# Performance work log

Measured on AMD Instinct MI355X. Metric: run time of the kernel, lower is better.

Reference implementation:

```python
import jax, jax.numpy as jnp
import numpy as np
from jax import lax

VOCAB = 1000
TMAX = 1001  # max_episode_length + 1
L = 2048
H_GRU = 256


def setup_inputs() -> dict:
    key = jax.random.key(0)
    ks = jax.random.split(key, 40)
    g = lambda i, shape, s: jax.random.normal(ks[i], shape, dtype=jnp.float32) * s
    inp = {
        "x": jax.random.normal(ks[0], (1, 3, 124, 124), dtype=jnp.float32),
        "curr_instr": jax.random.randint(ks[1], (1, L), 0, VOCAB),
        "prev_instr": jax.random.randint(ks[2], (1, L), 0, VOCAB),
        "next_instr": jax.random.randint(ks[3], (1, L), 0, VOCAB),
        "tx": jax.random.randint(ks[4], (1,), 0, TMAX),
        "hx": jnp.zeros((1, 768), jnp.float32),
        "cx": jnp.zeros((1, 768), jnp.float32),
        # conv stack
        "conv1_w": g(5, (128, 3, 8, 8), 0.05), "conv1_b": jnp.zeros((128,), jnp.float32),
        "conv2_w": g(6, (64, 128, 4, 4), 0.03), "conv2_b": jnp.zeros((64,), jnp.float32),
        "conv3_w": g(7, (64, 64, 4, 4), 0.03), "conv3_b": jnp.zeros((64,), jnp.float32),
        # embeddings
        "emb": g(8, (VOCAB, 32), 0.1),
        "time_emb": g(9, (TMAX, 32), 0.1),
        # GRU (torch nn.GRU layout: 3*H rows for r,z,n)
        "gru_w_ih": g(10, (3 * H_GRU, 32), 0.1), "gru_w_hh": g(11, (3 * H_GRU, H_GRU), 0.06),
        "gru_b_ih": jnp.zeros((3 * H_GRU,), jnp.float32), "gru_b_hh": jnp.zeros((3 * H_GRU,), jnp.float32),
        # attention linear 256 -> 64
        "attn_w": g(12, (64, H_GRU), 0.06), "attn_b": jnp.zeros((64,), jnp.float32),
        # image-fusion linear 64*6*6 -> 256
        "lin_w": g(13, (256, 64 * 6 * 6), 0.02), "lin_b": jnp.zeros((256,), jnp.float32),
        # LSTMCell 768 -> 768 (torch layout: 4*H rows for i,f,g,o)
        "lstm_w_ih": g(14, (4 * 768, 768), 0.03), "lstm_w_hh": g(15, (4 * 768, 768), 0.03),
        "lstm_b_ih": jnp.zeros((4 * 768,), jnp.float32), "lstm_b_hh": jnp.zeros((4 * 768,), jnp.float32),
        # heads over [hx, time_emb] = 768 + 32 = 800
        "critic_w": g(16, (1, 800), 0.03), "critic_b": jnp.zeros((1,), jnp.float32),
        "actor_w": g(17, (4, 800), 0.01), "actor_b": jnp.zeros((4,), jnp.float32),
    }
    return inp


def _conv(x, w, b, s):
    return lax.conv_general_dilated(x, w, (s, s), "VALID") + b[None, :, None, None]


def reference(x, curr_instr, prev_instr, next_instr, tx, hx, cx,
              conv1_w, conv1_b, conv2_w, conv2_b, conv3_w, conv3_b,
              emb, time_emb, gru_w_ih, gru_w_hh, gru_b_ih, gru_b_hh,
              attn_w, attn_b, lin_w, lin_b,
              lstm_w_ih, lstm_w_hh, lstm_b_ih, lstm_b_hh,
              critic_w, critic_b, actor_w, actor_b):
    # image tower: [1,3,124,124] -> [1,64,6,6]
    h1 = jax.nn.relu(_conv(x, conv1_w, conv1_b, 4))
    h2 = jax.nn.relu(_conv(h1, conv2_w, conv2_b, 2))
    x_image_rep = jax.nn.relu(_conv(h2, conv3_w, conv3_b, 2))

    # three instruction sequences, encoded by a shared GRU (vmapped scan)
    tokens = jnp.stack([curr_instr[0], prev_instr[0], next_instr[0]])  # [3, L]

    def gru_encode(tok):
        xs = emb[tok]                               # [L, 32]
        gi_all = xs @ gru_w_ih.T + gru_b_ih         # precompute input gates [L, 3H]
        def step(h, gi):
            gh = h @ gru_w_hh.T + gru_b_hh
            i_r, i_z, i_n = jnp.split(gi, 3)
            h_r, h_z, h_n = jnp.split(gh, 3)
            r = jax.nn.sigmoid(i_r + h_r)
            z = jax.nn.sigmoid(i_z + h_z)
            n = jnp.tanh(i_n + r * h_n)
            return (1.0 - z) * n + z * h, None
        h, _ = lax.scan(step, jnp.zeros((H_GRU,), xs.dtype), gi_all)
        return h

    h3 = jax.vmap(gru_encode)(tokens)               # [3, 256]
    attn = jax.nn.sigmoid(h3 @ attn_w.T + attn_b)   # [3, 64]

    # BUG-FAITHFUL: original forward uses cached_computation['curr_x_attention']
    # for all three branches, so the three fused features are identical.
    curr_attn = attn[0][None, :, None, None]        # [1,64,1,1]
    fused = (x_image_rep * curr_attn).reshape(1, -1)  # [1, 2304]
    feat = jax.nn.relu(fused @ lin_w.T + lin_b)     # [1, 256]
    xcat = jnp.concatenate([feat, feat, feat], axis=1)  # [1, 768]

    # LSTMCell
    gates = xcat @ lstm_w_ih.T + lstm_b_ih + hx @ lstm_w_hh.T + lstm_b_hh  # [1, 3072]
    gi, gf, gg, go = jnp.split(gates, 4, axis=1)
    cx_new = jax.nn.sigmoid(gf) * cx + jax.nn.sigmoid(gi) * jnp.tanh(gg)
    hx_new = jax.nn.sigmoid(go) * jnp.tanh(cx_new)

    t = time_emb[tx].reshape(-1, 32)                # [1, 32]
    z = jnp.concatenate([hx_new, t], axis=1)        # [1, 800]
    critic = z @ critic_w.T + critic_b              # [1, 1]
    actor = z @ actor_w.T + actor_b                 # [1, 4]
    return critic, actor, hx_new, cx_new
```

## Files before the change

kernel.cpp:

```cpp
#include <hip/hip_runtime.h>
#include <hip/hip_bf16.h>
#include <stdint.h>


typedef _Float16 half8 __attribute__((ext_vector_type(8)));
typedef _Float16 half2v __attribute__((ext_vector_type(2)));
typedef float f32x4 __attribute__((ext_vector_type(4)));

__device__ __forceinline__ float sigm(float x) { return 1.0f / (1.0f + __expf(-x)); }
__device__ __forceinline__ float tanh_f(float x) { return 2.0f / (1.0f + __expf(-2.0f * x)) - 1.0f; }

__global__ void k_pack(const float* __restrict__ whh, uint32_t* __restrict__ wf16p) {
    int i = blockIdx.x * 256 + threadIdx.x;
    if (i >= 98304) return;
    half2v p = {(_Float16)whh[2 * i], (_Float16)whh[2 * i + 1]};
    wf16p[i] = __builtin_bit_cast(uint32_t, p);
}

__global__ void k_conv1(const float* __restrict__ x, const float* __restrict__ w,
                        const float* __restrict__ b, float* __restrict__ h1) {
    int idx = blockIdx.x * 256 + threadIdx.x;
    if (idx >= 128 * 30 * 30) return;
    int ox = idx % 30, oy = (idx / 30) % 30, oc = idx / 900;
    const float* wr = w + oc * 192;
    float acc = b[oc];
    for (int c = 0; c < 3; ++c)
        for (int ky = 0; ky < 8; ++ky) {
            const float* xr = x + (c * 124 + oy * 4 + ky) * 124 + ox * 4;
            const float* wk = wr + (c * 8 + ky) * 8;
#pragma unroll
            for (int kx = 0; kx < 8; ++kx) acc = fmaf(xr[kx], wk[kx], acc);
        }
    h1[idx] = fmaxf(acc, 0.0f);
}

__global__ void k_conv2(const float* __restrict__ h1, const float* __restrict__ w,
                        const float* __restrict__ b, float* __restrict__ h2) {
    int idx = blockIdx.x * 256 + threadIdx.x;
    if (idx >= 64 * 14 * 14) return;
    int ox = idx % 14, oy = (idx / 14) % 14, oc = idx / 196;
    float acc = b[oc];
    const float* wr = w + oc * 128 * 16;
    for (int c = 0; c < 128; ++c) {
#pragma unroll
        for (int ky = 0; ky < 4; ++ky) {
            const float* hr = h1 + (c * 30 + oy * 2 + ky) * 30 + ox * 2;
            const float* wk = wr + (c * 4 + ky) * 4;
#pragma unroll
            for (int kx = 0; kx < 4; ++kx) acc = fmaf(hr[kx], wk[kx], acc);
        }
    }
    h2[idx] = fmaxf(acc, 0.0f);
}

__global__ void k_conv3(const float* __restrict__ h2, const float* __restrict__ w,
                        const float* __restrict__ b, float* __restrict__ x3) {
    int idx = blockIdx.x * 256 + threadIdx.x;
    if (idx >= 64 * 6 * 6) return;
    int ox = idx % 6, oy = (idx / 6) % 6, oc = idx / 36;
    float acc = b[oc];
    const float* wr = w + oc * 64 * 16;
    for (int c = 0; c < 64; ++c) {
#pragma unroll
        for (int ky = 0; ky < 4; ++ky) {
            const float* hr = h2 + (c * 14 + oy * 2 + ky) * 14 + ox * 2;
            const float* wk = wr + (c * 4 + ky) * 4;
#pragma unroll
            for (int kx = 0; kx < 4; ++kx) acc = fmaf(hr[kx], wk[kx], acc);
        }
    }
    x3[idx] = fmaxf(acc, 0.0f);
}

__global__ void k_gi(const int* __restrict__ curr, const float* __restrict__ emb,
                     const float* __restrict__ wih, const float* __restrict__ bih,
                     const float* __restrict__ bhh, float* __restrict__ gi) {
    int idx = blockIdx.x * 256 + threadIdx.x;
    int j = idx % 768, t = idx / 768;
    int tok = curr[t];
    const float4* e = (const float4*)(emb + tok * 32);
    const float4* wr = (const float4*)(wih + j * 32);
    float acc = bih[j] + (j < 512 ? bhh[j] : 0.0f);
#pragma unroll
    for (int k = 0; k < 8; ++k) {
        float4 ev = e[k], wv = wr[k];
        acc = fmaf(ev.x, wv.x, acc);
        acc = fmaf(ev.y, wv.y, acc);
        acc = fmaf(ev.z, wv.z, acc);
        acc = fmaf(ev.w, wv.w, acc);
    }
    gi[idx] = acc;
}

#define DECLBT(T) uint4 b##T##_0, b##T##_1, b##T##_2, b##T##_3, b##T##_4, b##T##_5, b##T##_6, b##T##_7;
#define LOADBK(T, kt, off) b##T##_##kt = wpR[(off) + (kt)*4 + quad];
#define LOADBT(T, off) LOADBK(T, 0, off) LOADBK(T, 1, off) LOADBK(T, 2, off) LOADBK(T, 3, off) \
                       LOADBK(T, 4, off) LOADBK(T, 5, off) LOADBK(T, 6, off) LOADBK(T, 7, off)
#define TIEBK(T, kt) \
    asm volatile("" : "+v"(b##T##_##kt.x), "+v"(b##T##_##kt.y), "+v"(b##T##_##kt.z), "+v"(b##T##_##kt.w));
#define TIEBT(T) TIEBK(T, 0) TIEBK(T, 1) TIEBK(T, 2) TIEBK(T, 3) TIEBK(T, 4) TIEBK(T, 5) TIEBK(T, 6) TIEBK(T, 7)
#define MF1(T, kt, areg) \
    acc##T = __builtin_amdgcn_mfma_f32_16x16x32_f16(areg, __builtin_bit_cast(half8, b##T##_##kt), acc##T, 0, 0, 0);
#define MFK(kt, areg) MF1(0, kt, areg) MF1(1, kt, areg) MF1(2, kt, areg) \
                      MF1(3, kt, areg) MF1(4, kt, areg) MF1(5, kt, areg)

__global__ __attribute__((amdgpu_flat_work_group_size(512, 512), amdgpu_waves_per_eu(2, 2)))
void k_gru_scan(const float* __restrict__ gi, const uint32_t* __restrict__ wf16p,
                const float* __restrict__ bhh, const float* __restrict__ attn_w,
                const float* __restrict__ attn_b, float* __restrict__ attn0) {
    __shared__ __align__(16) _Float16 hbuf[1024];
    const int tid = threadIdx.x;
    const int lane = tid & 63;
    const int wv = tid >> 6;
    const int n16 = lane & 15;
    const int quad = lane >> 4;
    const int li = n16;

    DECLBT(0) DECLBT(1) DECLBT(2) DECLBT(3) DECLBT(4) DECLBT(5)
    {
        const uint4* wpR = (const uint4*)wf16p + (size_t)(wv * 32 + n16) * 32;
        LOADBT(0, 0) LOADBT(1, 512) LOADBT(2, 8192) LOADBT(3, 8704) LOADBT(4, 16384) LOADBT(5, 16896)
    }
    TIEBT(0) TIEBT(1) TIEBT(2) TIEBT(3) TIEBT(4) TIEBT(5)

    const float bn0 = bhh[512 + wv * 32 + li];
    const float bn1 = bhh[512 + wv * 32 + 16 + li];
    float gr0, gr1, gz0, gz1, gn0v, gn1v;
    {
        const float* g0 = gi + wv * 32 + li;
        gr0 = g0[0]; gr1 = g0[16]; gz0 = g0[256]; gz1 = g0[272]; gn0v = g0[512]; gn1v = g0[528];
    }
    float h0 = 0.0f, h1 = 0.0f;
    hbuf[tid] = (_Float16)0.0f;
    hbuf[512 + tid] = (_Float16)0.0f;
    __syncthreads();

#pragma clang loop unroll(disable)
    for (int step = 0; step < 2048; ++step) {
        const uint4* ab = (const uint4*)hbuf + ((step & 1) << 6) + ((n16 == 1) ? 4 : 0);
        half8 aA = __builtin_bit_cast(half8, ab[0 * 8 + quad]);
        half8 aB = __builtin_bit_cast(half8, ab[1 * 8 + quad]);

        float pr0 = 0.f, pr1 = 0.f, pz0 = 0.f, pz1 = 0.f, pn0 = 0.f, pn1 = 0.f;
        if (step < 2047) {
            const float* gp = gi + (size_t)(step + 1) * 768 + wv * 32 + li;
            pr0 = gp[0]; pr1 = gp[16]; pz0 = gp[256]; pz1 = gp[272]; pn0 = gp[512]; pn1 = gp[528];
        }

        f32x4 acc0 = (f32x4)(0.0f), acc1 = (f32x4)(0.0f), acc2 = (f32x4)(0.0f);
        f32x4 acc3 = (f32x4)(0.0f), acc4 = (f32x4)(0.0f), acc5 = (f32x4)(0.0f);
        MFK(0, aA) aA = __builtin_bit_cast(half8, ab[2 * 8 + quad]);
        MFK(1, aB) aB = __builtin_bit_cast(half8, ab[3 * 8 + quad]);
        MFK(2, aA) aA = __builtin_bit_cast(half8, ab[4 * 8 + quad]);
        MFK(3, aB) aB = __builtin_bit_cast(half8, ab[5 * 8 + quad]);
        MFK(4, aA) aA = __builtin_bit_cast(half8, ab[6 * 8 + quad]);
        MFK(5, aB) aB = __builtin_bit_cast(half8, ab[7 * 8 + quad]);
        MFK(6, aA)
        MFK(7, aB)

        if (lane < 16) {
            const float SC = 0.0009765625f;
            float yr0 = fmaf(acc0.y, SC, acc0.x);
            float yr1 = fmaf(acc1.y, SC, acc1.x);
            float yz0 = fmaf(acc2.y, SC, acc2.x);
            float yz1 = fmaf(acc3.y, SC, acc3.x);
            float yn0 = fmaf(acc4.y, SC, acc4.x) + bn0;
            float yn1 = fmaf(acc5.y, SC, acc5.x) + bn1;
            float r0 = sigm(gr0 + yr0), r1 = sigm(gr1 + yr1);
            float z0 = sigm(gz0 + yz0), z1 = sigm(gz1 + yz1);
            float n0 = tanh_f(fmaf(r0, yn0, gn0v));
            float n1 = tanh_f(fmaf(r1, yn1, gn1v));
            h0 = fmaf(z0, h0 - n0, n0);
            h1 = fmaf(z1, h1 - n1, n1);
            int wb = (((step + 1) & 1) << 9) + (wv << 6);
            _Float16 h0h = (_Float16)h0, h1h = (_Float16)h1;
            hbuf[wb + li] = h0h;
            hbuf[wb + 32 + li] = (_Float16)((h0 - (float)h0h) * 1024.0f);
            hbuf[wb + 16 + li] = h1h;
            hbuf[wb + 48 + li] = (_Float16)((h1 - (float)h1h) * 1024.0f);
        }
        gr0 = pr0; gr1 = pr1; gz0 = pz0; gz1 = pz1; gn0v = pn0; gn1v = pn1;
        __syncthreads();
    }

    if (tid < 64) {
        const float* ar = attn_w + tid * 256;
        float acc = attn_b[tid];
        for (int k = 0; k < 256; ++k) {
            int c = k >> 5, i = k & 31;
            float hk = (float)hbuf[c * 64 + i] + (float)hbuf[c * 64 + 32 + i] * 0.0009765625f;
            acc = fmaf(ar[k], hk, acc);
        }
        attn0[tid] = sigm(acc);
    }
}

__global__ void k_feat(const float* __restrict__ x3, const float* __restrict__ attn0,
                       const float* __restrict__ lw, const float* __restrict__ lb,
                       float* __restrict__ feat) {
    __shared__ __align__(16) float fused[2304];
    int t = threadIdx.x;
    for (int i = t; i < 2304; i += 64) fused[i] = x3[i] * attn0[i / 36];
    __syncthreads();
    int row = blockIdx.x * 64 + t;
    const float4* wvv = (const float4*)(lw + (size_t)row * 2304);
    float acc = lb[row];
    for (int i = 0; i < 576; ++i) {
        float4 v = wvv[i];
        const float* f = fused + i * 4;
        acc = fmaf(v.x, f[0], acc);
        acc = fmaf(v.y, f[1], acc);
        acc = fmaf(v.z, f[2], acc);
        acc = fmaf(v.w, f[3], acc);
    }
    feat[row] = fmaxf(acc, 0.0f);
}

__global__ void k_lstm_gates(const float* __restrict__ wih, const float* __restrict__ whh,
                             const float* __restrict__ bih, const float* __restrict__ bhh,
                             const float* __restrict__ hx, const float* __restrict__ feat,
                             float* __restrict__ gates) {
    int wid = threadIdx.x >> 6, lane = threadIdx.x & 63;
    int row = blockIdx.x * 4 + wid;
    const float* wi = wih + (size_t)row * 768;
    const float* wh = whh + (size_t)row * 768;
    float acc = 0.0f;
#pragma unroll
    for (int i = 0; i < 12; ++i) {
        int k = lane + i * 64;
        acc = fmaf(wi[k], feat[k & 255], acc);
        acc = fmaf(wh[k], hx[k], acc);
    }
#pragma unroll
    for (int s = 32; s; s >>= 1) acc += __shfl_down(acc, s, 64);
    if (lane == 0) gates[row] = acc + bih[row] + bhh[row];
}

__global__ void k_lstm_cell(const float* __restrict__ gates, const float* __restrict__ cx,
                            float* __restrict__ out, float* __restrict__ hxf) {
    int i = threadIdx.x;
    float g_i = gates[i], g_f = gates[768 + i], g_g = gates[1536 + i], g_o = gates[2304 + i];
    float c = cx[i];
    float cn = sigm(g_f) * c + sigm(g_i) * tanh_f(g_g);
    float hn = sigm(g_o) * tanh_f(cn);
    out[5 + i] = hn;
    out[5 + 768 + i] = cn;
    hxf[i] = hn;
}

__global__ void k_heads(const float* __restrict__ hxf, const float* __restrict__ temb,
                        const int* __restrict__ tx, const float* __restrict__ cw,
                        const float* __restrict__ cb, const float* __restrict__ aw,
                        const float* __restrict__ ab, float* __restrict__ out) {
    __shared__ float z[800];
    int t = threadIdx.x;
    for (int i = t; i < 768; i += 320) z[i] = hxf[i];
    if (t < 32) z[768 + t] = temb[tx[0] * 32 + t];
    __syncthreads();
    int w = t >> 6, lane = t & 63;
    const float* row = (w == 0) ? cw : (aw + (size_t)(w - 1) * 800);
    float acc = 0.0f;
    for (int k = lane; k < 800; k += 64) acc = fmaf(row[k], z[k], acc);
#pragma unroll
    for (int s = 32; s; s >>= 1) acc += __shfl_down(acc, s, 64);
    if (lane == 0) {
        float b = (w == 0) ? cb[0] : ab[w - 1];
        out[w] = acc + b;
    }
}

extern "C" void kernel_launch(void* const* d_in, const int* in_sizes, int n_in,
                              void* d_out, int out_size, void* d_ws, size_t ws_size,
                              hipStream_t stream) {
    const float* x = (const float*)d_in[0];
    const int* curr = (const int*)d_in[1];
    const int* tx = (const int*)d_in[4];
    const float* hx = (const float*)d_in[5];
    const float* cx = (const float*)d_in[6];
    const float* c1w = (const float*)d_in[7];
    const float* c1b = (const float*)d_in[8];
    const float* c2w = (const float*)d_in[9];
    const float* c2b = (const float*)d_in[10];
    const float* c3w = (const float*)d_in[11];
    const float* c3b = (const float*)d_in[12];
    const float* emb = (const float*)d_in[13];
    const float* temb = (const float*)d_in[14];
    const float* gwih = (const float*)d_in[15];
    const float* gwhh = (const float*)d_in[16];
    const float* gbih = (const float*)d_in[17];
    const float* gbhh = (const float*)d_in[18];
    const float* attw = (const float*)d_in[19];
    const float* attb = (const float*)d_in[20];
    const float* linw = (const float*)d_in[21];
    const float* linb = (const float*)d_in[22];
    const float* lwih = (const float*)d_in[23];
    const float* lwhh = (const float*)d_in[24];
    const float* lbih = (const float*)d_in[25];
    const float* lbhh = (const float*)d_in[26];
    const float* cw = (const float*)d_in[27];
    const float* cb = (const float*)d_in[28];
    const float* aw = (const float*)d_in[29];
    const float* ab = (const float*)d_in[30];
    float* out = (float*)d_out;

    char* ws = (char*)d_ws;
    float* gi = (float*)(ws + 0);
    float* h1 = (float*)(ws + 6291456);
    float* h2 = (float*)(ws + 6752256);
    float* x3 = (float*)(ws + 6802432);
    float* attn0 = (float*)(ws + 6811648);
    float* feat = (float*)(ws + 6811904);
    float* gates = (float*)(ws + 6812928);
    float* hxf = (float*)(ws + 6825216);
    uint32_t* wf16p = (uint32_t*)(ws + 6828288);

    k_pack<<<384, 256, 0, stream>>>(gwhh, wf16p);
    k_gi<<<6144, 256, 0, stream>>>(curr, emb, gwih, gbih, gbhh, gi);
    k_conv1<<<450, 256, 0, stream>>>(x, c1w, c1b, h1);
    k_conv2<<<49, 256, 0, stream>>>(h1, c2w, c2b, h2);
    k_conv3<<<9, 256, 0, stream>>>(h2, c3w, c3b, x3);
    k_gru_scan<<<1, 512, 0, stream>>>(gi, wf16p, gbhh, attw, attb, attn0);
    k_feat<<<4, 64, 0, stream>>>(x3, attn0, linw, linb, feat);
    k_lstm_gates<<<768, 256, 0, stream>>>(lwih, lwhh, lbih, lbhh, hx, feat, gates);
    k_lstm_cell<<<1, 768, 0, stream>>>(gates, cx, out, hxf);
    k_heads<<<1, 320, 0, stream>>>(hxf, temb, tx, cw, cb, aw, ab, out);
}
```

Measured before the change: 2.671 ms.

## Split GRU scan across MFMA and dot2 waves; fold conv stack and packing into scan

The GRU recurrence is repartitioned so that four waves compute 128 hidden units with MFMA while the other four waves compute the remaining 128 units with packed fp16 dot2 instructions. Each wave's share of the recurrent matmul per step shrinks. The fp16 weight packing now happens in-kernel from the fp32 weights, which removes the separate pack kernel. The three conv kernels run inside a second block of the same launch, concurrently with the scan, which removes four launches. The risks are higher register pressure (48 uint4 per thread), a wave imbalance between the MFMA and dot2 paths, and a conv stack that is slow on a single block, though it overlaps the long scan.

```diff
diff --git a/kernel.cpp b/kernel.cpp
--- a/kernel.cpp
+++ b/kernel.cpp
@@ -9,68 +9,21 @@
 
 __device__ __forceinline__ float sigm(float x) { return 1.0f / (1.0f + __expf(-x)); }
 __device__ __forceinline__ float tanh_f(float x) { return 2.0f / (1.0f + __expf(-2.0f * x)) - 1.0f; }
-
-__global__ void k_pack(const float* __restrict__ whh, uint32_t* __restrict__ wf16p) {
-    int i = blockIdx.x * 256 + threadIdx.x;
-    if (i >= 98304) return;
-    half2v p = {(_Float16)whh[2 * i], (_Float16)whh[2 * i + 1]};
-    wf16p[i] = __builtin_bit_cast(uint32_t, p);
-}
-
-__global__ void k_conv1(const float* __restrict__ x, const float* __restrict__ w,
-                        const float* __restrict__ b, float* __restrict__ h1) {
-    int idx = blockIdx.x * 256 + threadIdx.x;
-    if (idx >= 128 * 30 * 30) return;
-    int ox = idx % 30, oy = (idx / 30) % 30, oc = idx / 900;
-    const float* wr = w + oc * 192;
-    float acc = b[oc];
-    for (int c = 0; c < 3; ++c)
-        for (int ky = 0; ky < 8; ++ky) {
-            const float* xr = x + (c * 124 + oy * 4 + ky) * 124 + ox * 4;
-            const float* wk = wr + (c * 8 + ky) * 8;
-#pragma unroll
-            for (int kx = 0; kx < 8; ++kx) acc = fmaf(xr[kx], wk[kx], acc);
-        }
-    h1[idx] = fmaxf(acc, 0.0f);
-}
-
-__global__ void k_conv2(const float* __restrict__ h1, const float* __restrict__ w,
-                        const float* __restrict__ b, float* __restrict__ h2) {
-    int idx = blockIdx.x * 256 + threadIdx.x;
-    if (idx >= 64 * 14 * 14) return;
-    int ox = idx % 14, oy = (idx / 14) % 14, oc = idx / 196;
-    float acc = b[oc];
-    const float* wr = w + oc * 128 * 16;
-    for (int c = 0; c < 128; ++c) {
-#pragma unroll
-        for (int ky = 0; ky < 4; ++ky) {
-            const float* hr = h1 + (c * 30 + oy * 2 + ky) * 30 + ox * 2;
-            const float* wk = wr + (c * 4 + ky) * 4;
-#pragma unroll
-            for (int kx = 0; kx < 4; ++kx) acc = fmaf(hr[kx], wk[kx], acc);
-        }
-    }
-    h2[idx] = fmaxf(acc, 0.0f);
-}
-
-__global__ void k_conv3(const float* __restrict__ h2, const float* __restrict__ w,
-                        const float* __restrict__ b, float* __restrict__ x3) {
-    int idx = blockIdx.x * 256 + threadIdx.x;
-    if (idx >= 64 * 6 * 6) return;
-    int ox = idx % 6, oy = (idx / 6) % 6, oc = idx / 36;
-    float acc = b[oc];
-    const float* wr = w + oc * 64 * 16;
-    for (int c = 0; c < 64; ++c) {
-#pragma unroll
-        for (int ky = 0; ky < 4; ++ky) {
-            const float* hr = h2 + (c * 14 + oy * 2 + ky) * 14 + ox * 2;
-            const float* wk = wr + (c * 4 + ky) * 4;
-#pragma unroll
-            for (int kx = 0; kx < 4; ++kx) acc = fmaf(hr[kx], wk[kx], acc);
-        }
-    }
-    x3[idx] = fmaxf(acc, 0.0f);
-}
+__device__ __forceinline__ uint32_t pk(float a, float b) {
+    half2v h = {(_Float16)a, (_Float16)b};
+    return __builtin_bit_cast(uint32_t, h);
+}
+#if __has_builtin(__builtin_amdgcn_fdot2)
+__device__ __forceinline__ float dot2(uint32_t w, uint32_t h, float acc) {
+    return __builtin_amdgcn_fdot2(__builtin_bit_cast(half2v, w),
+                                  __builtin_bit_cast(half2v, h), acc, false);
+}
+#else
+__device__ __forceinline__ float dot2(uint32_t w, uint32_t h, float acc) {
+    half2v wv = __builtin_bit_cast(half2v, w), hv = __builtin_bit_cast(half2v, h);
+    return fmaf((float)wv.y, (float)hv.y, fmaf((float)wv.x, (float)hv.x, acc));
+}
+#endif
 
 __global__ void k_gi(const int* __restrict__ curr, const float* __restrict__ emb,
                      const float* __restrict__ wih, const float* __restrict__ bih,
@@ -92,94 +45,270 @@
     gi[idx] = acc;
 }
 
-#define DECLBT(T) uint4 b##T##_0, b##T##_1, b##T##_2, b##T##_3, b##T##_4, b##T##_5, b##T##_6, b##T##_7;
-#define LOADBK(T, kt, off) b##T##_##kt = wpR[(off) + (kt)*4 + quad];
-#define LOADBT(T, off) LOADBK(T, 0, off) LOADBK(T, 1, off) LOADBK(T, 2, off) LOADBK(T, 3, off) \
-                       LOADBK(T, 4, off) LOADBK(T, 5, off) LOADBK(T, 6, off) LOADBK(T, 7, off)
-#define TIEBK(T, kt) \
-    asm volatile("" : "+v"(b##T##_##kt.x), "+v"(b##T##_##kt.y), "+v"(b##T##_##kt.z), "+v"(b##T##_##kt.w));
-#define TIEBT(T) TIEBK(T, 0) TIEBK(T, 1) TIEBK(T, 2) TIEBK(T, 3) TIEBK(T, 4) TIEBK(T, 5) TIEBK(T, 6) TIEBK(T, 7)
-#define MF1(T, kt, areg) \
-    acc##T = __builtin_amdgcn_mfma_f32_16x16x32_f16(areg, __builtin_bit_cast(half8, b##T##_##kt), acc##T, 0, 0, 0);
-#define MFK(kt, areg) MF1(0, kt, areg) MF1(1, kt, areg) MF1(2, kt, areg) \
-                      MF1(3, kt, areg) MF1(4, kt, areg) MF1(5, kt, areg)
+#define REPU(X) X(0) X(1) X(2) X(3) X(4) X(5) X(6) X(7) X(8) X(9) X(10) X(11)   \
+    X(12) X(13) X(14) X(15) X(16) X(17) X(18) X(19) X(20) X(21) X(22) X(23)     \
+    X(24) X(25) X(26) X(27) X(28) X(29) X(30) X(31) X(32) X(33) X(34) X(35)     \
+    X(36) X(37) X(38) X(39) X(40) X(41) X(42) X(43) X(44) X(45) X(46) X(47)
+#define DECLU(i) uint4 U##i;
+#define TIEU(i) asm volatile("" : "+v"(U##i.x), "+v"(U##i.y), "+v"(U##i.z), "+v"(U##i.w));
+#define PACK8(dst, p)                                  \
+    {                                                  \
+        float4 fA = *(const float4*)(p);               \
+        float4 fB = *(const float4*)((p) + 4);         \
+        dst.x = pk(fA.x, fA.y); dst.y = pk(fA.z, fA.w); \
+        dst.z = pk(fB.x, fB.y); dst.w = pk(fB.z, fB.w); \
+    }
+#define PACKT(u0, u1, u2, u3, u4, u5, u6, u7, rp)                        \
+    PACK8(u0, (rp) + 0 * 32 + quad * 8) PACK8(u1, (rp) + 1 * 32 + quad * 8) \
+    PACK8(u2, (rp) + 2 * 32 + quad * 8) PACK8(u3, (rp) + 3 * 32 + quad * 8) \
+    PACK8(u4, (rp) + 4 * 32 + quad * 8) PACK8(u5, (rp) + 5 * 32 + quad * 8) \
+    PACK8(u6, (rp) + 6 * 32 + quad * 8) PACK8(u7, (rp) + 7 * 32 + quad * 8)
+#define MM(A, B, C) __builtin_amdgcn_mfma_f32_16x16x32_f16(A, __builtin_bit_cast(half8, B), C, 0, 0, 0)
+#define MF6(A, u0, u1, u2, u3, u4, u5)                           \
+    acc0 = MM(A, u0, acc0); acc1 = MM(A, u1, acc1);              \
+    acc2 = MM(A, u2, acc2); acc3 = MM(A, u3, acc3);              \
+    acc4 = MM(A, u4, acc4); acc5 = MM(A, u5, acc5);
+#define CHUNK(cc, A0, A1, A2, A3, B0, B1)                                          \
+    {                                                                              \
+        uint4 hh0 = hb[cc * 8 + 0], hh1 = hb[cc * 8 + 1];                          \
+        uint4 hh2 = hb[cc * 8 + 2], hh3 = hb[cc * 8 + 3];                          \
+        uint4 hl0 = hb[cc * 8 + 4], hl1 = hb[cc * 8 + 5];                          \
+        uint4 hl2 = hb[cc * 8 + 6], hl3 = hb[cc * 8 + 7];                          \
+        uint4 bh0 = hb[cc * 8 + hoff], bh1 = hb[cc * 8 + hoff + 1];                \
+        uint4 bl0 = hb[cc * 8 + hoff + 4], bl1 = hb[cc * 8 + hoff + 5];            \
+        accAH = dot2(A0.x, hh0.x, accAH); accAH = dot2(A0.y, hh0.y, accAH);        \
+        accAH = dot2(A0.z, hh0.z, accAH); accAH = dot2(A0.w, hh0.w, accAH);        \
+        accAH = dot2(A1.x, hh1.x, accAH); accAH = dot2(A1.y, hh1.y, accAH);        \
+        accAH = dot2(A1.z, hh1.z, accAH); accAH = dot2(A1.w, hh1.w, accAH);        \
+        accAH = dot2(A2.x, hh2.x, accAH); accAH = dot2(A2.y, hh2.y, accAH);        \
+        accAH = dot2(A2.z, hh2.z, accAH); accAH = dot2(A2.w, hh2.w, accAH);        \
+        accAH = dot2(A3.x, hh3.x, accAH); accAH = dot2(A3.y, hh3.y, accAH);        \
+        accAH = dot2(A3.z, hh3.z, accAH); accAH = dot2(A3.w, hh3.w, accAH);        \
+        accAL = dot2(A0.x, hl0.x, accAL); accAL = dot2(A0.y, hl0.y, accAL);        \
+        accAL = dot2(A0.z, hl0.z, accAL); accAL = dot2(A0.w, hl0.w, accAL);        \
+        accAL = dot2(A1.x, hl1.x, accAL); accAL = dot2(A1.y, hl1.y, accAL);        \
+        accAL = dot2(A1.z, hl1.z, accAL); accAL = dot2(A1.w, hl1.w, accAL);        \
+        accAL = dot2(A2.x, hl2.x, accAL); accAL = dot2(A2.y, hl2.y, accAL);        \
+        accAL = dot2(A2.z, hl2.z, accAL); accAL = dot2(A2.w, hl2.w, accAL);        \
+        accAL = dot2(A3.x, hl3.x, accAL); accAL = dot2(A3.y, hl3.y, accAL);        \
+        accAL = dot2(A3.z, hl3.z, accAL); accAL = dot2(A3.w, hl3.w, accAL);        \
+        accBH = dot2(B0.x, bh0.x, accBH); accBH = dot2(B0.y, bh0.y, accBH);        \
+        accBH = dot2(B0.z, bh0.z, accBH); accBH = dot2(B0.w, bh0.w, accBH);        \
+        accBH = dot2(B1.x, bh1.x, accBH); accBH = dot2(B1.y, bh1.y, accBH);        \
+        accBH = dot2(B1.z, bh1.z, accBH); accBH = dot2(B1.w, bh1.w, accBH);        \
+        accBL = dot2(B0.x, bl0.x, accBL); accBL = dot2(B0.y, bl0.y, accBL);        \
+        accBL = dot2(B0.z, bl0.z, accBL); accBL = dot2(B0.w, bl0.w, accBL);        \
+        accBL = dot2(B1.x, bl1.x, accBL); accBL = dot2(B1.y, bl1.y, accBL);        \
+        accBL = dot2(B1.z, bl1.z, accBL); accBL = dot2(B1.w, bl1.w, accBL);        \
+    }
 
 __global__ __attribute__((amdgpu_flat_work_group_size(512, 512), amdgpu_waves_per_eu(2, 2)))
-void k_gru_scan(const float* __restrict__ gi, const uint32_t* __restrict__ wf16p,
-                const float* __restrict__ bhh, const float* __restrict__ attn_w,
-                const float* __restrict__ attn_b, float* __restrict__ attn0) {
-    __shared__ __align__(16) _Float16 hbuf[1024];
+void k_scan(const float* __restrict__ gi, const float* __restrict__ whh,
+            const float* __restrict__ bhh, const float* __restrict__ attn_w,
+            const float* __restrict__ attn_b, float* __restrict__ attn0,
+            const float* __restrict__ x, const float* __restrict__ c1w,
+            const float* __restrict__ c1b, const float* __restrict__ c2w,
+            const float* __restrict__ c2b, const float* __restrict__ c3w,
+            const float* __restrict__ c3b, float* __restrict__ h1,
+            float* __restrict__ h2, float* __restrict__ x3) {
+    const int bid = blockIdx.x;
     const int tid = threadIdx.x;
+
+    if (bid == 1) {
+        for (int it = 0; it < 225; ++it) {
+            int idx = it * 512 + tid;
+            int ox = idx % 30, oy = (idx / 30) % 30, oc = idx / 900;
+            const float* wr = c1w + oc * 192;
+            float acc = c1b[oc];
+            for (int c = 0; c < 3; ++c)
+                for (int ky = 0; ky < 8; ++ky) {
+                    const float* xr = x + (c * 124 + oy * 4 + ky) * 124 + ox * 4;
+                    const float* wk = wr + (c * 8 + ky) * 8;
+#pragma unroll
+                    for (int kx = 0; kx < 8; ++kx) acc = fmaf(xr[kx], wk[kx], acc);
+                }
+            h1[idx] = fmaxf(acc, 0.0f);
+        }
+        __syncthreads();
+        for (int it = 0; it < 25; ++it) {
+            int idx = it * 512 + tid;
+            if (idx < 12544) {
+                int ox = idx % 14, oy = (idx / 14) % 14, oc = idx / 196;
+                float acc = c2b[oc];
+                const float* wr = c2w + oc * 128 * 16;
+                for (int c = 0; c < 128; ++c) {
+#pragma unroll
+                    for (int ky = 0; ky < 4; ++ky) {
+                        const float* hr = h1 + (c * 30 + oy * 2 + ky) * 30 + ox * 2;
+                        const float* wk = wr + (c * 4 + ky) * 4;
+#pragma unroll
+                        for (int kx = 0; kx < 4; ++kx) acc = fmaf(hr[kx], wk[kx], acc);
+                    }
+                }
+                h2[idx] = fmaxf(acc, 0.0f);
+            }
+        }
+        __syncthreads();
+        for (int it = 0; it < 5; ++it) {
+            int idx = it * 512 + tid;
+            if (idx < 2304) {
+                int ox = idx % 6, oy = (idx / 6) % 6, oc = idx / 36;
+                float acc = c3b[oc];
+                const float* wr = c3w + oc * 64 * 16;
+                for (int c = 0; c < 64; ++c) {
+#pragma unroll
+                    for (int ky = 0; ky < 4; ++ky) {
+                        const float* hr = h2 + (c * 14 + oy * 2 + ky) * 14 + ox * 2;
+                        const float* wk = wr + (c * 4 + ky) * 4;
+#pragma unroll
+                        for (int kx = 0; kx < 4; ++kx) acc = fmaf(hr[kx], wk[kx], acc);
+                    }
+                }
+                x3[idx] = fmaxf(acc, 0.0f);
+            }
+        }
+        return;
+    }
+
     const int lane = tid & 63;
     const int wv = tid >> 6;
     const int n16 = lane & 15;
     const int quad = lane >> 4;
-    const int li = n16;
-
-    DECLBT(0) DECLBT(1) DECLBT(2) DECLBT(3) DECLBT(4) DECLBT(5)
-    {
-        const uint4* wpR = (const uint4*)wf16p + (size_t)(wv * 32 + n16) * 32;
-        LOADBT(0, 0) LOADBT(1, 512) LOADBT(2, 8192) LOADBT(3, 8704) LOADBT(4, 16384) LOADBT(5, 16896)
-    }
-    TIEBT(0) TIEBT(1) TIEBT(2) TIEBT(3) TIEBT(4) TIEBT(5)
-
-    const float bn0 = bhh[512 + wv * 32 + li];
-    const float bn1 = bhh[512 + wv * 32 + 16 + li];
-    float gr0, gr1, gz0, gz1, gn0v, gn1v;
-    {
-        const float* g0 = gi + wv * 32 + li;
-        gr0 = g0[0]; gr1 = g0[16]; gz0 = g0[256]; gz1 = g0[272]; gn0v = g0[512]; gn1v = g0[528];
-    }
-    float h0 = 0.0f, h1 = 0.0f;
+    const bool mfmaw = (wv < 4);
+
+    __shared__ __align__(16) _Float16 hbuf[1024];
+
+    REPU(DECLU)
+    float gr0 = 0.f, gr1 = 0.f, gz0 = 0.f, gz1 = 0.f, gn0 = 0.f, gn1 = 0.f;
+    float bn0 = 0.f, bn1 = 0.f;
+    float h0 = 0.f, h1r = 0.f;
+    const int hoff = ((lane >> 5) & 1) * 2;
+
+    if (mfmaw) {
+        const float* rp0 = whh + (size_t)(wv * 32 + n16) * 256;
+        const float* rp1 = whh + (size_t)(wv * 32 + 16 + n16) * 256;
+        const float* rp2 = whh + (size_t)(256 + wv * 32 + n16) * 256;
+        const float* rp3 = whh + (size_t)(256 + wv * 32 + 16 + n16) * 256;
+        const float* rp4 = whh + (size_t)(512 + wv * 32 + n16) * 256;
+        const float* rp5 = whh + (size_t)(512 + wv * 32 + 16 + n16) * 256;
+        PACKT(U0, U1, U2, U3, U4, U5, U6, U7, rp0)
+        PACKT(U8, U9, U10, U11, U12, U13, U14, U15, rp1)
+        PACKT(U16, U17, U18, U19, U20, U21, U22, U23, rp2)
+        PACKT(U24, U25, U26, U27, U28, U29, U30, U31, rp3)
+        PACKT(U32, U33, U34, U35, U36, U37, U38, U39, rp4)
+        PACKT(U40, U41, U42, U43, U44, U45, U46, U47, rp5)
+        bn0 = bhh[512 + wv * 32 + n16];
+        bn1 = bhh[512 + wv * 32 + 16 + n16];
+        if (lane < 16) {
+            const float* gp = gi + wv * 32 + n16;
+            gr0 = gp[0]; gr1 = gp[16]; gz0 = gp[256]; gz1 = gp[272];
+            gn0 = gp[512]; gn1 = gp[528];
+        }
+    } else {
+        const int e = 128 + (wv - 4) * 32 + (lane & 31);
+        const int rowA = (lane < 32) ? e : (256 + e);
+        const int ksub = (lane < 32) ? 0 : 16;
+        const float* rowAp = whh + (size_t)rowA * 256;
+        const float* rowNp = whh + (size_t)(512 + e) * 256;
+#define PA(a) PACK8(U##a, rowAp + a * 8)
+        PA(0) PA(1) PA(2) PA(3) PA(4) PA(5) PA(6) PA(7)
+        PA(8) PA(9) PA(10) PA(11) PA(12) PA(13) PA(14) PA(15)
+        PA(16) PA(17) PA(18) PA(19) PA(20) PA(21) PA(22) PA(23)
+        PA(24) PA(25) PA(26) PA(27) PA(28) PA(29) PA(30) PA(31)
+#define PB(b, c, q) PACK8(U##b, rowNp + (c) * 32 + ksub + (q) * 8)
+        PB(32, 0, 0) PB(33, 0, 1) PB(34, 1, 0) PB(35, 1, 1)
+        PB(36, 2, 0) PB(37, 2, 1) PB(38, 3, 0) PB(39, 3, 1)
+        PB(40, 4, 0) PB(41, 4, 1) PB(42, 5, 0) PB(43, 5, 1)
+        PB(44, 6, 0) PB(45, 6, 1) PB(46, 7, 0) PB(47, 7, 1)
+        bn0 = bhh[512 + e];
+        if (lane < 32) {
+            const float* gp = gi + e;
+            gr0 = gp[0]; gz0 = gp[256]; gn0 = gp[512];
+        }
+    }
+    REPU(TIEU)
+
     hbuf[tid] = (_Float16)0.0f;
     hbuf[512 + tid] = (_Float16)0.0f;
     __syncthreads();
 
 #pragma clang loop unroll(disable)
     for (int step = 0; step < 2048; ++step) {
-        const uint4* ab = (const uint4*)hbuf + ((step & 1) << 6) + ((n16 == 1) ? 4 : 0);
-        half8 aA = __builtin_bit_cast(half8, ab[0 * 8 + quad]);
-        half8 aB = __builtin_bit_cast(half8, ab[1 * 8 + quad]);
-
-        float pr0 = 0.f, pr1 = 0.f, pz0 = 0.f, pz1 = 0.f, pn0 = 0.f, pn1 = 0.f;
-        if (step < 2047) {
-            const float* gp = gi + (size_t)(step + 1) * 768 + wv * 32 + li;
-            pr0 = gp[0]; pr1 = gp[16]; pz0 = gp[256]; pz1 = gp[272]; pn0 = gp[512]; pn1 = gp[528];
-        }
-
-        f32x4 acc0 = (f32x4)(0.0f), acc1 = (f32x4)(0.0f), acc2 = (f32x4)(0.0f);
-        f32x4 acc3 = (f32x4)(0.0f), acc4 = (f32x4)(0.0f), acc5 = (f32x4)(0.0f);
-        MFK(0, aA) aA = __builtin_bit_cast(half8, ab[2 * 8 + quad]);
-        MFK(1, aB) aB = __builtin_bit_cast(half8, ab[3 * 8 + quad]);
-        MFK(2, aA) aA = __builtin_bit_cast(half8, ab[4 * 8 + quad]);
-        MFK(3, aB) aB = __builtin_bit_cast(half8, ab[5 * 8 + quad]);
-        MFK(4, aA) aA = __builtin_bit_cast(half8, ab[6 * 8 + quad]);
-        MFK(5, aB) aB = __builtin_bit_cast(half8, ab[7 * 8 + quad]);
-        MFK(6, aA)
-        MFK(7, aB)
-
-        if (lane < 16) {
+        const int par = step & 1;
+        const int wb = ((step + 1) & 1) * 512 + wv * 64;
+        if (mfmaw) {
+            const uint4* ab = (const uint4*)hbuf + par * 64 + ((n16 == 1) ? 4 : 0);
+            half8 aA = __builtin_bit_cast(half8, ab[0 * 8 + quad]);
+            half8 aB = __builtin_bit_cast(half8, ab[1 * 8 + quad]);
+            float pr0 = 0.f, pr1 = 0.f, pz0 = 0.f, pz1 = 0.f, pn0 = 0.f, pn1 = 0.f;
+            if (step < 2047 && lane < 16) {
+                const float* gp = gi + (size_t)(step + 1) * 768 + wv * 32 + n16;
+                pr0 = gp[0]; pr1 = gp[16]; pz0 = gp[256]; pz1 = gp[272];
+                pn0 = gp[512]; pn1 = gp[528];
+            }
+            f32x4 acc0 = (f32x4)(0.f), acc1 = (f32x4)(0.f), acc2 = (f32x4)(0.f);
+            f32x4 acc3 = (f32x4)(0.f), acc4 = (f32x4)(0.f), acc5 = (f32x4)(0.f);
+            MF6(aA, U0, U8, U16, U24, U32, U40) aA = __builtin_bit_cast(half8, ab[2 * 8 + quad]);
+            MF6(aB, U1, U9, U17, U25, U33, U41) aB = __builtin_bit_cast(half8, ab[3 * 8 + quad]);
+            MF6(aA, U2, U10, U18, U26, U34, U42) aA = __builtin_bit_cast(half8, ab[4 * 8 + quad]);
+            MF6(aB, U3, U11, U19, U27, U35, U43) aB = __builtin_bit_cast(half8, ab[5 * 8 + quad]);
+            MF6(aA, U4, U12, U20, U28, U36, U44) aA = __builtin_bit_cast(half8, ab[6 * 8 + quad]);
+            MF6(aB, U5, U13, U21, U29, U37, U45) aB = __builtin_bit_cast(half8, ab[7 * 8 + quad]);
+            MF6(aA, U6, U14, U22, U30, U38, U46)
+            MF6(aB, U7, U15, U23, U31, U39, U47)
+            if (lane < 16) {
+                const float SC = 0.0009765625f;
+                float yr0 = fmaf(acc0.y, SC, acc0.x);
+                float yr1 = fmaf(acc1.y, SC, acc1.x);
+                float yz0 = fmaf(acc2.y, SC, acc2.x);
+                float yz1 = fmaf(acc3.y, SC, acc3.x);
+                float yn0 = fmaf(acc4.y, SC, acc4.x) + bn0;
+                float yn1 = fmaf(acc5.y, SC, acc5.x) + bn1;
+                float r0 = sigm(gr0 + yr0), r1 = sigm(gr1 + yr1);
+                float z0 = sigm(gz0 + yz0), z1 = sigm(gz1 + yz1);
+                float n0 = tanh_f(fmaf(r0, yn0, gn0));
+                float n1 = tanh_f(fmaf(r1, yn1, gn1));
+                h0 = fmaf(z0, h0 - n0, n0);
+                h1r = fmaf(z1, h1r - n1, n1);
+                _Float16 h0h = (_Float16)h0, h1h = (_Float16)h1r;
+                hbuf[wb + n16] = h0h;
+                hbuf[wb + 32 + n16] = (_Float16)((h0 - (float)h0h) * 1024.0f);
+                hbuf[wb + 16 + n16] = h1h;
+                hbuf[wb + 48 + n16] = (_Float16)((h1r - (float)h1h) * 1024.0f);
+            }
+            gr0 = pr0; gr1 = pr1; gz0 = pz0; gz1 = pz1; gn0 = pn0; gn1 = pn1;
+        } else {
+            const uint4* hb = (const uint4*)hbuf + par * 64;
+            float pr0 = 0.f, pz0 = 0.f, pn0 = 0.f;
+            if (step < 2047 && lane < 32) {
+                const float* gp = gi + (size_t)(step + 1) * 768 + 128 + (wv - 4) * 32 + lane;
+                pr0 = gp[0]; pz0 = gp[256]; pn0 = gp[512];
+            }
+            float accAH = 0.f, accAL = 0.f, accBH = 0.f, accBL = 0.f;
+            CHUNK(0, U0, U1, U2, U3, U32, U33)
+            CHUNK(1, U4, U5, U6, U7, U34, U35)
+            CHUNK(2, U8, U9, U10, U11, U36, U37)
+            CHUNK(3, U12, U13, U14, U15, U38, U39)
+            CHUNK(4, U16, U17, U18, U19, U40, U41)
+            CHUNK(5, U20, U21, U22, U23, U42, U43)
+            CHUNK(6, U24, U25, U26, U27, U44, U45)
+            CHUNK(7, U28, U29, U30, U31, U46, U47)
             const float SC = 0.0009765625f;
-            float yr0 = fmaf(acc0.y, SC, acc0.x);
-            float yr1 = fmaf(acc1.y, SC, acc1.x);
-            float yz0 = fmaf(acc2.y, SC, acc2.x);
-            float yz1 = fmaf(acc3.y, SC, acc3.x);
-            float yn0 = fmaf(acc4.y, SC, acc4.x) + bn0;
-            float yn1 = fmaf(acc5.y, SC, acc5.x) + bn1;
-            float r0 = sigm(gr0 + yr0), r1 = sigm(gr1 + yr1);
-            float z0 = sigm(gz0 + yz0), z1 = sigm(gz1 + yz1);
-            float n0 = tanh_f(fmaf(r0, yn0, gn0v));
-            float n1 = tanh_f(fmaf(r1, yn1, gn1v));
-            h0 = fmaf(z0, h0 - n0, n0);
-            h1 = fmaf(z1, h1 - n1, n1);
-            int wb = (((step + 1) & 1) << 9) + (wv << 6);
-            _Float16 h0h = (_Float16)h0, h1h = (_Float16)h1;
-            hbuf[wb + li] = h0h;
-            hbuf[wb + 32 + li] = (_Float16)((h0 - (float)h0h) * 1024.0f);
-            hbuf[wb + 16 + li] = h1h;
-            hbuf[wb + 48 + li] = (_Float16)((h1 - (float)h1h) * 1024.0f);
-        }
-        gr0 = pr0; gr1 = pr1; gz0 = pz0; gz1 = pz1; gn0v = pn0; gn1v = pn1;
+            float ad = fmaf(accAL, SC, accAH);
+            float bd = fmaf(accBL, SC, accBH);
+            float zd = __shfl_xor(ad, 32);
+            float nd = bd + __shfl_xor(bd, 32);
+            if (lane < 32) {
+                float r = sigm(gr0 + ad);
+                float z = sigm(gz0 + zd);
+                float n = tanh_f(fmaf(r, nd + bn0, gn0));
+                h0 = fmaf(z, h0 - n, n);
+                _Float16 hh = (_Float16)h0;
+                hbuf[wb + lane] = hh;
+                hbuf[wb + 32 + lane] = (_Float16)((h0 - (float)hh) * 1024.0f);
+            }
+            gr0 = pr0; gz0 = pz0; gn0 = pn0;
+        }
         __syncthreads();
     }
 
@@ -312,14 +441,10 @@
     float* feat = (float*)(ws + 6811904);
     float* gates = (float*)(ws + 6812928);
     float* hxf = (float*)(ws + 6825216);
-    uint32_t* wf16p = (uint32_t*)(ws + 6828288);
-
-    k_pack<<<384, 256, 0, stream>>>(gwhh, wf16p);
+
     k_gi<<<6144, 256, 0, stream>>>(curr, emb, gwih, gbih, gbhh, gi);
-    k_conv1<<<450, 256, 0, stream>>>(x, c1w, c1b, h1);
-    k_conv2<<<49, 256, 0, stream>>>(h1, c2w, c2b, h2);
-    k_conv3<<<9, 256, 0, stream>>>(h2, c3w, c3b, x3);
-    k_gru_scan<<<1, 512, 0, stream>>>(gi, wf16p, gbhh, attw, attb, attn0);
+    k_scan<<<2, 512, 0, stream>>>(gi, gwhh, gbhh, attw, attb, attn0,
+                                  x, c1w, c1b, c2w, c2b, c3w, c3b, h1, h2, x3);
     k_feat<<<4, 64, 0, stream>>>(x3, attn0, linw, linb, feat);
     k_lstm_gates<<<768, 256, 0, stream>>>(lwih, lwhh, lbih, lbhh, hx, feat, gates);
     k_lstm_cell<<<1, 768, 0, stream>>>(gates, cx, out, hxf);
```

New measurement: 4.686 ms. 75.5% more time.
